# Kernel tuning notes

Hardware: AMD Instinct MI355X
Metric: run time of the kernel (lower is better)

Reference implementation:

```python
import jax, jax.numpy as jnp
import numpy as np
from jax import lax

CONV_SIZE = 5
MORPH_SIZE = 5
TH1_INIT = 0.5
STEP = 0.0005
LO, HI = 0.84, 0.86


def _maxpool(a):
    p = MORPH_SIZE // 2
    return lax.reduce_window(
        a, -jnp.inf, lax.max,
        window_dimensions=(1, 1, MORPH_SIZE, MORPH_SIZE),
        window_strides=(1, 1, 1, 1),
        padding=[(0, 0), (0, 0), (p, p), (p, p)])


def setup_inputs() -> dict:
    key = jax.random.key(0)
    k1, _ = jax.random.split(key)
    x = jax.random.uniform(k1, (8, 4, 1024, 1024), dtype=jnp.float32)
    blur_k = jnp.full((1, 1, CONV_SIZE, CONV_SIZE), 1.0 / CONV_SIZE ** 2, dtype=jnp.float32)
    return {"x": x, "blur_k": blur_k}


def reference(x, blur_k):
    N, c, h, w = x.shape
    xi = x.reshape(N * c, 1, h, w)
    out = lax.conv_general_dilated(
        xi, blur_k, window_strides=(1, 1), padding='SAME',
        dimension_numbers=('NCHW', 'OIHW', 'NCHW')).reshape(N, c, h, w)

    # iterative mean-based threshold (quantile) search, same as the torch while-loops
    out_c = lax.stop_gradient(out)

    def frac_above(th):
        return jnp.mean(jnp.where(out_c > th, 1.0, 0.0))

    th = jnp.float32(TH1_INIT)
    th = lax.while_loop(lambda t: frac_above(t) < LO, lambda t: t - STEP, th)
    th = lax.while_loop(lambda t: frac_above(t) > HI, lambda t: t + STEP, th)

    thr = jnp.where(out > th, 1.0, 0.0)
    # morphological close: max-pool then min-pool (min = -maxpool(-x))
    closed = -_maxpool(-_maxpool(thr))
    return closed  # torch casts to float64; kept float32 (see notes)
```

## Files before the change

kernel.cpp:

```cpp
#include <hip/hip_runtime.h>


#define K_STEPS 1024
#define LO_COUNT 28185723u
#define R_TILE 16
#define PT_ROWS 16

#define OFF_HIST 4096
#define OFF_KQ   16384

typedef float  fx4 __attribute__((ext_vector_type(4)));

struct TTable { float v[K_STEPS]; };
static constexpr TTable make_T() {
    TTable t{};
    float th = 0.5f;
    for (int k = 0; k < K_STEPS; k++) { t.v[k] = th; th = th - 0.0005f; }
    return t;
}
__device__ constexpr TTable Tc = make_T();

__device__ __forceinline__ uint4 cvt4(float4 f) {
    return make_uint4((unsigned int)(f.x * 8388608.0f),
                      (unsigned int)(f.y * 8388608.0f),
                      (unsigned int)(f.z * 8388608.0f),
                      (unsigned int)(f.w * 8388608.0f));
}

__device__ __forceinline__ int find_ki(const unsigned int* __restrict__ Us,
                                       float gbias, unsigned int s) {
    float g = fmaf(-(float)s, 9.5367432e-6f, gbias);
    int lo = (int)g;
    lo = max(0, min(1022, lo));
    unsigned int a0 = Us[lo], a1 = Us[lo + 1];
    return lo + (int)(s < a0) + (int)(s < a1);
}

__global__ __launch_bounds__(256, 6) void
k_pass1(const float4* __restrict__ x4, const float* __restrict__ bk,
        unsigned int* __restrict__ hist, unsigned short* __restrict__ kq16) {
    __shared__ unsigned int Us[K_STEPS];
    __shared__ unsigned int lh[K_STEPS + 1];
    int tid = threadIdx.x;
    int p = blockIdx.y, y0 = blockIdx.x * R_TILE;
    int wlane = tid & 63;

    {
        double c = (double)bk[0] * (1.0 / 8388608.0);
        #pragma unroll
        for (int i = 0; i < 4; i++) {
            int k = tid + 256 * i;
            double T = (double)Tc.v[k];
            unsigned int u = 0u;
            if (T >= 0.0) {
                u = (unsigned int)(floor(T / c) + 1.0);
                while (u > 0u && (double)(u - 1u) * c > T) u--;
                while (!((double)u * c > T)) u++;
            }
            Us[k] = u;
        }
    }
    for (int i = tid; i < K_STEPS + 1; i += 256) lh[i] = 0u;
    __syncthreads();
    float gbias = fmaf((float)Us[0], 9.5367432e-6f, 0.5f);

    const float4* pf = x4 + (size_t)p * 262144;
    int tB = (tid < 255) ? tid + 1 : 0;
    const uint4 z4 = make_uint4(0u, 0u, 0u, 0u);
    bool edge = (wlane == 63);

    unsigned int cs0 = 0, cs1 = 0, cs2 = 0, cs3 = 0;
    unsigned int cb0 = 0, cb1 = 0, cb2 = 0, cb3 = 0;
    {
        float4 ra[5], rb[5];
        #pragma unroll
        for (int i = 0; i < 5; i++) {
            int yy = y0 - 2 + i, yc = min(max(yy, 0), 1023);
            ra[i] = pf[yc * 256 + tid];
            if (edge) rb[i] = pf[yc * 256 + tB];
        }
        #pragma unroll
        for (int i = 0; i < 5; i++) {
            bool v = (unsigned)(y0 - 2 + i) < 1024u;
            uint4 a = v ? cvt4(ra[i]) : z4;
            cs0 += a.x; cs1 += a.y; cs2 += a.z; cs3 += a.w;
            if (edge) {
                uint4 b = v ? cvt4(rb[i]) : z4;
                cb0 += b.x; cb1 += b.y; cb2 += b.z; cb3 += b.w;
            }
        }
    }

    unsigned int cnt0 = 0;
    #pragma unroll 4
    for (int iy = 0; iy < R_TILE; iy++) {
        int y = y0 + iy;

        int yn = min(y + 3, 1023), yo = max(y - 2, 0);
        float4 Na = pf[yn * 256 + tid];
        float4 Oa = pf[yo * 256 + tid];
        float4 Nb, Ob;
        if (edge) { Nb = pf[yn * 256 + tB]; Ob = pf[yo * 256 + tB]; }

        unsigned int nc0 = __shfl_down(cs0, 1);
        unsigned int nc1 = __shfl_down(cs1, 1);
        unsigned int nc2 = __shfl_down(cs2, 1);
        unsigned int nc3 = __shfl_down(cs3, 1);
        if (edge) { nc0 = cb0; nc1 = cb1; nc2 = cb2; nc3 = cb3; }

        unsigned int m123 = cs1 + cs2 + cs3;
        unsigned int h45  = nc0 + nc1;
        unsigned int v0, v1, v2, v3;
        if (tid != 255) {
            v0 = cs0 + m123 + nc0;
            v1 = m123 + h45;
            v2 = cs2 + cs3 + h45 + nc2;
            v3 = cs3 + h45 + nc2 + nc3;
        } else {
            v0 = cs0 + m123;
            v1 = m123;
            v2 = h45 + nc2;
            v3 = h45 + nc2 + nc3;
        }

        int k0 = find_ki(Us, gbias, v0);
        int k1 = find_ki(Us, gbias, v1);
        int k2 = find_ki(Us, gbias, v2);
        int k3 = find_ki(Us, gbias, v3);
        cnt0 += (unsigned)(k0 == 0) + (unsigned)(k1 == 0)
              + (unsigned)(k2 == 0) + (unsigned)(k3 == 0);
        if (k0 > 0) atomicAdd(&lh[k0], 1u);
        if (k1 > 0) atomicAdd(&lh[k1], 1u);
        if (k2 > 0) atomicAdd(&lh[k2], 1u);
        if (k3 > 0) atomicAdd(&lh[k3], 1u);

        unsigned int pa = (unsigned)min(k0, 255) | ((unsigned)min(k1, 255) << 8);
        unsigned int pb = (unsigned)min(k2, 255) | ((unsigned)min(k3, 255) << 8);
        unsigned int paN = __shfl_down(pa, 1);
        size_t rb = ((size_t)p * 1024 + (size_t)y) * 512;
        if (wlane < 63) {
            ((unsigned int*)(kq16 + rb))[tid + 1] = pb | (paN << 16);
        } else {
            kq16[rb + ((tid < 255) ? (unsigned)(2 * tid + 2) : 0u)] =
                (unsigned short)pb;
        }
        if (wlane == 0) kq16[rb + 2 * tid + 1] = (unsigned short)pa;

        {
            bool vn = (unsigned)(y + 3) < 1024u;
            bool vo = (y - 2) >= 0;
            uint4 na = vn ? cvt4(Na) : z4;
            uint4 oa = vo ? cvt4(Oa) : z4;
            cs0 += na.x - oa.x; cs1 += na.y - oa.y;
            cs2 += na.z - oa.z; cs3 += na.w - oa.w;
            if (edge) {
                uint4 nb = vn ? cvt4(Nb) : z4;
                uint4 ob = vo ? cvt4(Ob) : z4;
                cb0 += nb.x - ob.x; cb1 += nb.y - ob.y;
                cb2 += nb.z - ob.z; cb3 += nb.w - ob.w;
            }
        }
    }

    #pragma unroll
    for (int d = 32; d > 0; d >>= 1) cnt0 += __shfl_down(cnt0, d);
    if ((tid & 63) == 0 && cnt0) atomicAdd(&lh[0], cnt0);
    __syncthreads();
    for (int i = tid; i < K_STEPS + 1; i += 256) {
        unsigned int c = lh[i];
        if (c) atomicAdd(&hist[i], c);
    }
}

__global__ __launch_bounds__(256, 6) void
k_post(const unsigned char* __restrict__ kqb, const unsigned int* __restrict__ hist,
       float* __restrict__ out) {
    __shared__ unsigned long long Tt[24 * 16];
    __shared__ unsigned long long Vv[20 * 16];
    __shared__ unsigned long long Dd[20 * 16];
    __shared__ unsigned long long Ww[16 * 16];
    __shared__ unsigned long long Ff[16 * 16];
    __shared__ int ksS;

    int tid = threadIdx.x;
    int p = blockIdx.y, y0 = blockIdx.x * PT_ROWS;

    const unsigned char* kp = kqb + (size_t)p * 1048576;
    uint4 q0, q1, q2, q3, q4, q5;
    {
        const uint4 zq = make_uint4(0u, 0u, 0u, 0u);
        #pragma unroll
        for (int i = 0; i < 6; i++) {
            int ch = tid + 256 * i;
            int r = ch >> 6, cc = ch & 63;
            int pr = y0 - 4 + r;
            uint4 q = zq;
            if ((unsigned)pr < 1024u)
                q = ((const uint4*)(kp + (size_t)pr * 1024))[cc];
            if (i == 0) q0 = q; else if (i == 1) q1 = q;
            else if (i == 2) q2 = q; else if (i == 3) q3 = q;
            else if (i == 4) q4 = q; else q5 = q;
        }
    }

    if (tid < 64) {
        int lane = tid;
        unsigned int h[16], s = 0;
        #pragma unroll
        for (int i = 0; i < 16; i++) { h[i] = hist[lane * 16 + i]; s += h[i]; }
        unsigned int inc = s;
        #pragma unroll
        for (int d = 1; d < 64; d <<= 1) {
            unsigned int t = __shfl_up(inc, d);
            if (lane >= d) inc += t;
        }
        unsigned int excl = inc - s;
        bool cross = (excl < LO_COUNT) && (excl + s >= LO_COUNT);
        unsigned long long m = __ballot(cross);
        if (m) {
            int cl = __ffsll((long long)m) - 1;
            if (lane == cl) {
                unsigned int c = excl; int ks = K_STEPS - 1;
                for (int i = 0; i < 16; i++) { c += h[i]; if (c >= LO_COUNT) { ks = lane * 16 + i; break; } }
                ksS = ks;
            }
        } else if (lane == 0) ksS = K_STEPS - 1;
    }
    __syncthreads();
    int ks = ksS;

    unsigned short* Tt16 = (unsigned short*)Tt;
    #pragma unroll
    for (int i = 0; i < 6; i++) {
        uint4 q = (i == 0) ? q0 : (i == 1) ? q1 : (i == 2) ? q2
                : (i == 3) ? q3 : (i == 4) ? q4 : q5;
        int ch = tid + 256 * i;
        int r = ch >> 6;
        int pr = y0 - 4 + r;
        unsigned int m = 0u;
        unsigned int wv;
        wv = q.x;
        m |= (unsigned)((wv & 0xffu) <= (unsigned)ks)
           | ((unsigned)(((wv >> 8) & 0xffu) <= (unsigned)ks) << 1)
           | ((unsigned)(((wv >> 16) & 0xffu) <= (unsigned)ks) << 2)
           | ((unsigned)((wv >> 24) <= (unsigned)ks) << 3);
        wv = q.y;
        m |= ((unsigned)((wv & 0xffu) <= (unsigned)ks) << 4)
           | ((unsigned)(((wv >> 8) & 0xffu) <= (unsigned)ks) << 5)
           | ((unsigned)(((wv >> 16) & 0xffu) <= (unsigned)ks) << 6)
           | ((unsigned)((wv >> 24) <= (unsigned)ks) << 7);
        wv = q.z;
        m |= ((unsigned)((wv & 0xffu) <= (unsigned)ks) << 8)
           | ((unsigned)(((wv >> 8) & 0xffu) <= (unsigned)ks) << 9)
           | ((unsigned)(((wv >> 16) & 0xffu) <= (unsigned)ks) << 10)
           | ((unsigned)((wv >> 24) <= (unsigned)ks) << 11);
        wv = q.w;
        m |= ((unsigned)((wv & 0xffu) <= (unsigned)ks) << 12)
           | ((unsigned)(((wv >> 8) & 0xffu) <= (unsigned)ks) << 13)
           | ((unsigned)(((wv >> 16) & 0xffu) <= (unsigned)ks) << 14)
           | ((unsigned)((wv >> 24) <= (unsigned)ks) << 15);
        if ((unsigned)pr >= 1024u) m = 0u;
        Tt16[ch] = (unsigned short)m;
    }
    __syncthreads();

    for (int i = tid; i < 320; i += 256) {
        int vr = i >> 4, wc = i & 15;
        int b = vr * 16 + wc;
        Vv[i] = Tt[b] | Tt[b + 16] | Tt[b + 32] | Tt[b + 48] | Tt[b + 64];
    }
    __syncthreads();

    for (int i = tid; i < 320; i += 256) {
        int vr = i >> 4, wc = i & 15;
        int pr = y0 - 2 + vr;
        if ((unsigned)pr >= 1024u) { Dd[i] = ~0ull; continue; }
        unsigned long long Vc = Vv[i];
        unsigned long long Vl = (wc > 0)  ? Vv[i - 1] : 0ull;
        unsigned long long Vr = (wc < 15) ? Vv[i + 1] : 0ull;
        Dd[i] = Vc
            | (Vc << 1) | (Vl >> 63)
            | (Vc << 2) | (Vl >> 62)
            | (Vc >> 1) | (Vr << 63)
            | (Vc >> 2) | (Vr << 62);
    }
    __syncthreads();

    {
        int wr = tid >> 4, wc = tid & 15;
        int b = wr * 16 + wc;
        Ww[tid] = Dd[b] & Dd[b + 16] & Dd[b + 32] & Dd[b + 48] & Dd[b + 64];
    }
    __syncthreads();

    {
        int wc = tid & 15;
        unsigned long long Wc = Ww[tid];
        unsigned long long Wl = (wc > 0)  ? Ww[tid - 1] : ~0ull;
        unsigned long long Wr = (wc < 15) ? Ww[tid + 1] : ~0ull;
        Ff[tid] = Wc
            & ((Wc << 1) | (Wl >> 63))
            & ((Wc << 2) | (Wl >> 62))
            & ((Wc >> 1) | (Wr << 63))
            & ((Wc >> 2) | (Wr << 62));
    }
    __syncthreads();

    for (int i = 0; i < PT_ROWS; i++) {
        unsigned long long wd = Ff[i * 16 + (tid >> 4)];
        int sh = (tid & 15) * 4;
        fx4 f;
        f.x = (float)((wd >> sh) & 1ull);
        f.y = (float)((wd >> (sh + 1)) & 1ull);
        f.z = (float)((wd >> (sh + 2)) & 1ull);
        f.w = (float)((wd >> (sh + 3)) & 1ull);
        fx4* dst = (fx4*)(out + (size_t)p * 1048576 + (size_t)(y0 + i) * 1024) + tid;
        __builtin_nontemporal_store(f, dst);
    }
}

extern "C" void kernel_launch(void* const* d_in, const int* in_sizes, int n_in,
                              void* d_out, int out_size, void* d_ws, size_t ws_size,
                              hipStream_t stream) {
    const float4* x4 = (const float4*)d_in[0];
    const float*  bk = (const float*)d_in[1];
    float* out = (float*)d_out;

    char* ws = (char*)d_ws;
    unsigned int*   hist = (unsigned int*)(ws + OFF_HIST);
    unsigned short* kq16 = (unsigned short*)(ws + OFF_KQ);
    const unsigned char* kqb = (const unsigned char*)(ws + OFF_KQ);

    (void)hipMemsetAsync(hist, 0, (K_STEPS + 1) * sizeof(unsigned int), stream);

    dim3 g1(1024 / R_TILE, 32);
    k_pass1<<<g1, 256, 0, stream>>>(x4, bk, hist, kq16);

    dim3 g2(1024 / PT_ROWS, 32);
    k_post<<<g2, 256, 0, stream>>>(kqb, hist, out);
}
```

Measured before the change: 289.1 us.

## Stage converted input rows in an LDS ring buffer to avoid re-reading old rows

The sliding vertical box-sum in k_pass1 used to load two rows per output row from global memory, the incoming row and the outgoing row. It now keeps an 11-slot shared-memory ring of already-converted fixed-point rows, prefetching each new row about 8 rows ahead. This roughly halves global loads per output row, drops one cvt4 per row, and gives load latency more time to hide. In exchange it uses about 44KB of extra LDS and lowers the launch-bounds occupancy hint from 6 to 3 blocks.

```diff
diff --git a/kernel.cpp b/kernel.cpp
--- a/kernel.cpp
+++ b/kernel.cpp
@@ -36,14 +36,17 @@
     return lo + (int)(s < a0) + (int)(s < a1);
 }
 
-__global__ __launch_bounds__(256, 6) void
+__global__ __launch_bounds__(256, 3) void
 k_pass1(const float4* __restrict__ x4, const float* __restrict__ bk,
         unsigned int* __restrict__ hist, unsigned short* __restrict__ kq16) {
     __shared__ unsigned int Us[K_STEPS];
     __shared__ unsigned int lh[K_STEPS + 1];
+    __shared__ uint4 RA[11][256];
+    __shared__ uint4 RB[11][4];
     int tid = threadIdx.x;
     int p = blockIdx.y, y0 = blockIdx.x * R_TILE;
     int wlane = tid & 63;
+    int w = tid >> 6;
 
     {
         double c = (double)bk[0] * (1.0 / 8388608.0);
@@ -72,35 +75,33 @@
     unsigned int cs0 = 0, cs1 = 0, cs2 = 0, cs3 = 0;
     unsigned int cb0 = 0, cb1 = 0, cb2 = 0, cb3 = 0;
     {
-        float4 ra[5], rb[5];
-        #pragma unroll
-        for (int i = 0; i < 5; i++) {
+        #pragma unroll
+        for (int i = 0; i < 10; i++) {
             int yy = y0 - 2 + i, yc = min(max(yy, 0), 1023);
-            ra[i] = pf[yc * 256 + tid];
-            if (edge) rb[i] = pf[yc * 256 + tB];
-        }
-        #pragma unroll
-        for (int i = 0; i < 5; i++) {
-            bool v = (unsigned)(y0 - 2 + i) < 1024u;
-            uint4 a = v ? cvt4(ra[i]) : z4;
-            cs0 += a.x; cs1 += a.y; cs2 += a.z; cs3 += a.w;
+            bool v = (unsigned)yy < 1024u;
+            float4 ra = pf[yc * 256 + tid];
+            uint4 a = v ? cvt4(ra) : z4;
+            RA[i][tid] = a;
+            if (i < 5) { cs0 += a.x; cs1 += a.y; cs2 += a.z; cs3 += a.w; }
             if (edge) {
-                uint4 b = v ? cvt4(rb[i]) : z4;
-                cb0 += b.x; cb1 += b.y; cb2 += b.z; cb3 += b.w;
+                float4 rb = pf[yc * 256 + tB];
+                uint4 b = v ? cvt4(rb) : z4;
+                RB[i][w] = b;
+                if (i < 5) { cb0 += b.x; cb1 += b.y; cb2 += b.z; cb3 += b.w; }
             }
         }
     }
 
     unsigned int cnt0 = 0;
+    int sSub = 0, sAdd = 5, sWr = 10;
     #pragma unroll 4
     for (int iy = 0; iy < R_TILE; iy++) {
         int y = y0 + iy;
 
-        int yn = min(y + 3, 1023), yo = max(y - 2, 0);
-        float4 Na = pf[yn * 256 + tid];
-        float4 Oa = pf[yo * 256 + tid];
-        float4 Nb, Ob;
-        if (edge) { Nb = pf[yn * 256 + tB]; Ob = pf[yo * 256 + tB]; }
+        int yn = min(y + 8, 1023);
+        float4 Nf = pf[yn * 256 + tid];
+        float4 NfB;
+        if (edge) NfB = pf[yn * 256 + tB];
 
         unsigned int nc0 = __shfl_down(cs0, 1);
         unsigned int nc1 = __shfl_down(cs1, 1);
@@ -147,19 +148,27 @@
         if (wlane == 0) kq16[rb + 2 * tid + 1] = (unsigned short)pa;
 
         {
-            bool vn = (unsigned)(y + 3) < 1024u;
-            bool vo = (y - 2) >= 0;
-            uint4 na = vn ? cvt4(Na) : z4;
-            uint4 oa = vo ? cvt4(Oa) : z4;
+            uint4 na = RA[sAdd][tid];
+            uint4 oa = RA[sSub][tid];
             cs0 += na.x - oa.x; cs1 += na.y - oa.y;
             cs2 += na.z - oa.z; cs3 += na.w - oa.w;
             if (edge) {
-                uint4 nb = vn ? cvt4(Nb) : z4;
-                uint4 ob = vo ? cvt4(Ob) : z4;
+                uint4 nb = RB[sAdd][w];
+                uint4 ob = RB[sSub][w];
                 cb0 += nb.x - ob.x; cb1 += nb.y - ob.y;
                 cb2 += nb.z - ob.z; cb3 += nb.w - ob.w;
             }
         }
+
+        {
+            bool vw = (unsigned)(y + 8) < 1024u;
+            RA[sWr][tid] = vw ? cvt4(Nf) : z4;
+            if (edge) RB[sWr][w] = vw ? cvt4(NfB) : z4;
+        }
+
+        sSub++; if (sSub == 11) sSub = 0;
+        sAdd++; if (sAdd == 11) sAdd = 0;
+        sWr++;  if (sWr == 11)  sWr = 0;
     }
 
     #pragma unroll
```

Result: slower. 325.7 us (+12.7%).
